# Kernel tuning notes

Hardware: AMD Instinct MI355X
Metric: run time of the kernel (lower is better)

The kernel has to match this reference:

```python
import jax, jax.numpy as jnp
import numpy as np

N_NODES = 50000
N_EDGES = 1600000
IN_DIM = 128
HID = 64
N_GRAPHS = 256


def gcn_conv(x, row, col, W, b, n_nodes):
    """PyG GCNConv: symmetric gcn_norm with self-loops, linear-then-aggregate."""
    h = x @ W  # [N, out]
    loop = jnp.arange(n_nodes, dtype=row.dtype)
    r = jnp.concatenate([row, loop])  # sources (messages from x[r])
    c = jnp.concatenate([col, loop])  # targets (aggregate at c)
    ew = jnp.ones(r.shape[0], dtype=x.dtype)
    deg = jax.ops.segment_sum(ew, c, num_segments=n_nodes)
    dinv = jnp.where(deg > 0, jax.lax.rsqrt(deg), 0.0).astype(x.dtype)
    norm = dinv[r] * dinv[c]  # [E+N]
    out = jax.ops.segment_sum(norm[:, None] * h[r], c, num_segments=n_nodes)
    return out + b


def global_mean_pool(x, batch, n_graphs):
    sums = jax.ops.segment_sum(x, batch, num_segments=n_graphs)
    cnt = jax.ops.segment_sum(jnp.ones(x.shape[0], x.dtype), batch, num_segments=n_graphs)
    return sums / jnp.clip(cnt, 1.0)[:, None]


def setup_inputs() -> dict:
    key = jax.random.key(0)
    ks = jax.random.split(key, 12)
    x = jax.random.normal(ks[0], (N_NODES, IN_DIM), dtype=jnp.float32)
    edge_index = jax.random.randint(ks[1], (2, N_EDGES), 0, N_NODES, dtype=jnp.int64)
    batch = jnp.sort(jax.random.randint(ks[2], (N_NODES,), 0, N_GRAPHS, dtype=jnp.int64))
    def glorot(k, shp):
        lim = float(np.sqrt(6.0 / (shp[0] + shp[1])))
        return jax.random.uniform(k, shp, jnp.float32, -lim, lim)
    return {
        "x": x,
        "edge_index": edge_index,
        "batch": batch,
        "W1": glorot(ks[3], (IN_DIM, HID)), "b1": jnp.zeros((HID,), jnp.float32),
        "W2": glorot(ks[4], (HID, HID)), "b2": jnp.zeros((HID,), jnp.float32),
        "W3": glorot(ks[5], (HID, HID)), "b3": jnp.zeros((HID,), jnp.float32),
        "Wl1": glorot(ks[6], (HID, 16)), "bl1": jnp.zeros((16,), jnp.float32),
        "Wl2": glorot(ks[7], (16, 1)), "bl2": jnp.zeros((1,), jnp.float32),
    }


def reference(x, edge_index, batch, W1, b1, W2, b2, W3, b3, Wl1, bl1, Wl2, bl2):
    n = x.shape[0]
    row, col = edge_index[0], edge_index[1]
    h = jax.nn.relu(gcn_conv(x, row, col, W1, b1, n))
    h = jax.nn.relu(gcn_conv(h, row, col, W2, b2, n))
    h = jax.nn.relu(gcn_conv(h, row, col, W3, b3, n))
    g = global_mean_pool(h, batch, N_GRAPHS)  # [G, 64]
    out = (g @ Wl1 + bl1) @ Wl2 + bl2  # [G, 1]
    return out
```

## Files before the change

### kernel.cpp

```cpp
#include <hip/hip_runtime.h>

#define HID 64
#define B1 256
#define NBMAX 200
#define CAP 10368

typedef __attribute__((ext_vector_type(8))) short short8;
typedef __attribute__((ext_vector_type(4))) float float4v;

__device__ __forceinline__ ushort f2bf(float f) {
  unsigned u = __float_as_uint(f);
  unsigned r = (u + 0x7fffu + ((u >> 16) & 1u)) >> 16;
  return (ushort)r;
}
__device__ __forceinline__ float bf2f(ushort v) {
  return __uint_as_float(((unsigned)v) << 16);
}
__device__ __forceinline__ float4 up4(ushort4 v) {
  float4 r;
  r.x = bf2f(v.x);
  r.y = bf2f(v.y);
  r.z = bf2f(v.z);
  r.w = bf2f(v.w);
  return r;
}


__global__ __launch_bounds__(256) void bucket_hist(const int* __restrict__ col, int E, int epb,
                                                   int* __restrict__ buckettot,
                                                   const float* __restrict__ W1,
                                                   const float* __restrict__ W2,
                                                   const float* __restrict__ W3,
                                                   ushort* __restrict__ Wt1h, ushort* __restrict__ Wt1l,
                                                   ushort* __restrict__ Wt2h, ushort* __restrict__ Wt2l,
                                                   ushort* __restrict__ Wt3h, ushort* __restrict__ Wt3l) {
  int b = blockIdx.x, t = threadIdx.x;
  int gt = b * 256 + t;
  if (gt < 128 * 64) {
    int k = gt >> 6, nn = gt & 63;
    float w = W1[gt];
    ushort h = f2bf(w);
    Wt1h[nn * 128 + k] = h;
    Wt1l[nn * 128 + k] = f2bf(w - bf2f(h));
  }
  if (gt < 64 * 64) {
    int k = gt >> 6, nn = gt & 63;
    float w2 = W2[gt], w3 = W3[gt];
    ushort h2 = f2bf(w2), h3 = f2bf(w3);
    Wt2h[nn * 64 + k] = h2;
    Wt2l[nn * 64 + k] = f2bf(w2 - bf2f(h2));
    Wt3h[nn * 64 + k] = h3;
    Wt3l[nn * 64 + k] = f2bf(w3 - bf2f(h3));
  }

  __shared__ int cnt[256];
  cnt[t] = 0;
  __syncthreads();
  int lo = b * epb, hi = min(lo + epb, E);
  for (int e = lo + t; e < hi; e += 256) atomicAdd(&cnt[col[e] >> 8], 1);
  __syncthreads();
  int v = cnt[t];
  if (v > 0) atomicAdd(&buckettot[t], v);
}

__global__ __launch_bounds__(256) void scan_buckettot(const int* __restrict__ buckettot,
                                                      int* __restrict__ bucketbase,
                                                      int* __restrict__ woffglob,
                                                      int* __restrict__ csr_off, int n, int E,
                                                      int nb) {
  __shared__ int s[256];
  int t = threadIdx.x;
  int v = (t < nb) ? buckettot[t] : 0;
  s[t] = v;
  __syncthreads();
  for (int d = 1; d < 256; d <<= 1) {
    int u = (t >= d) ? s[t - d] : 0;
    __syncthreads();
    s[t] += u;
    __syncthreads();
  }
  int base = (t == 0) ? 0 : s[t - 1];
  if (t <= nb) bucketbase[t] = base;
  woffglob[t] = base;
  if (t == 0) csr_off[n] = E;
}

__global__ __launch_bounds__(256) void bin_edges(const int* __restrict__ row,
                                                 const int* __restrict__ col, int E, int epb,
                                                 int* __restrict__ woffglob,
                                                 unsigned* __restrict__ binned) {
  __shared__ int cnt[256];
  __shared__ int ofs[256];
  __shared__ int gb[256];
  __shared__ int lcur[256];
  __shared__ unsigned stage[4096];
  int b = blockIdx.x, t = threadIdx.x;
  int lo = b * epb, hi = min(lo + epb, E);

  for (int bs = lo; bs < hi; bs += 4096) {
    int ecnt = min(4096, hi - bs);
    cnt[t] = 0;
    __syncthreads();
    for (int i = t; i < ecnt; i += 256) atomicAdd(&cnt[col[bs + i] >> 8], 1);
    __syncthreads();
    int v = cnt[t];
    ofs[t] = v;
    __syncthreads();
    for (int d = 1; d < 256; d <<= 1) {
      int u = (t >= d) ? ofs[t - d] : 0;
      __syncthreads();
      ofs[t] += u;
      __syncthreads();
    }
    int excl = ofs[t] - v;
    int g = 0;
    if (v > 0) g = atomicAdd(&woffglob[t], v);
    __syncthreads();
    ofs[t] = excl;
    gb[t] = g;
    lcur[t] = excl;
    __syncthreads();
    for (int i = t; i < ecnt; i += 256) {
      int c = col[bs + i];
      int r = row[bs + i];
      int p = atomicAdd(&lcur[c >> 8], 1);
      stage[p] = ((unsigned)r << 16) | (unsigned)c;
    }
    __syncthreads();
    for (int i = t; i < ecnt; i += 256) {
      unsigned en = stage[i];
      int bb = (en >> 8) & 255;
      binned[gb[bb] + (i - ofs[bb])] = en;
    }
    __syncthreads();
  }
}

__global__ __launch_bounds__(256) void bucket_csr(const unsigned* __restrict__ binned,
                                                  const int* __restrict__ bucketbase,
                                                  int* __restrict__ csr_off,
                                                  int* __restrict__ csr_src,
                                                  float* __restrict__ dinv, int n) {
  __shared__ int lcnt[256];
  __shared__ int lofs[256];
  __shared__ int lsrc[CAP];
  int k = blockIdx.x, t = threadIdx.x;
  int base = bucketbase[k], end = bucketbase[k + 1];
  int s = end - base;
  lcnt[t] = 0;
  __syncthreads();
  for (int i = t; i < s; i += 256) {
    unsigned p = binned[base + i];
    atomicAdd(&lcnt[p & 255u], 1);
  }
  __syncthreads();
  int v = lcnt[t];
  lofs[t] = v;
  __syncthreads();
  for (int d = 1; d < 256; d <<= 1) {
    int u = (t >= d) ? lofs[t - d] : 0;
    __syncthreads();
    lofs[t] += u;
    __syncthreads();
  }
  int excl = lofs[t] - v;
  int node = (k << 8) + t;
  if (node < n) {
    csr_off[node] = base + excl;
    dinv[node] = rsqrtf((float)(v + 1));
  }
  lcnt[t] = excl;
  __syncthreads();
  for (int i = t; i < s; i += 256) {
    unsigned p = binned[base + i];
    int pos = atomicAdd(&lcnt[p & 255u], 1);
    if (pos < CAP) lsrc[pos] = (int)(p >> 16);
  }
  __syncthreads();
  for (int i = t; i < s; i += 256) csr_src[base + i] = (i < CAP) ? lsrc[i] : 0;
}


template <int K>
__global__ __launch_bounds__(256) void gemm_mfma(const float* __restrict__ A,
                                                 const ushort* __restrict__ Wh,
                                                 const ushort* __restrict__ Wl,
                                                 const float* __restrict__ dinv,
                                                 ushort* __restrict__ out, int n) {
  int wave = (blockIdx.x * 256 + threadIdx.x) >> 6;
  int lane = threadIdx.x & 63;
  int row0 = wave * 16;
  if (row0 >= n) return;
  int m = lane & 15;
  int quad = lane >> 4;
  int r = row0 + m;
  int rc = (r < n) ? r : (n - 1);

  float4v acc[4];
#pragma unroll
  for (int t = 0; t < 4; ++t) acc[t] = (float4v){0.f, 0.f, 0.f, 0.f};

#pragma unroll
  for (int k0 = 0; k0 < K; k0 += 32) {
    const float4* xp = (const float4*)&A[(size_t)rc * K + k0 + quad * 8];
    float4 a0 = xp[0];
    float4 a1 = xp[1];
    float av[8] = {a0.x, a0.y, a0.z, a0.w, a1.x, a1.y, a1.z, a1.w};
    short8 ah, al;
#pragma unroll
    for (int i = 0; i < 8; ++i) {
      ushort h = f2bf(av[i]);
      ah[i] = (short)h;
      al[i] = (short)f2bf(av[i] - bf2f(h));
    }
#pragma unroll
    for (int t = 0; t < 4; ++t) {
      size_t wof = (size_t)(t * 16 + m) * K + k0 + quad * 8;
      short8 bh = *(const short8*)&Wh[wof];
      short8 bl = *(const short8*)&Wl[wof];
      acc[t] = __builtin_amdgcn_mfma_f32_16x16x32_bf16(ah, bh, acc[t], 0, 0, 0);
      acc[t] = __builtin_amdgcn_mfma_f32_16x16x32_bf16(al, bh, acc[t], 0, 0, 0);
      acc[t] = __builtin_amdgcn_mfma_f32_16x16x32_bf16(ah, bl, acc[t], 0, 0, 0);
    }
  }

  float4 dv = ((const float4*)dinv)[(row0 >> 2) + quad];
  float dvi[4] = {dv.x, dv.y, dv.z, dv.w};
#pragma unroll
  for (int i = 0; i < 4; ++i) {
    int orow = row0 + quad * 4 + i;
    if (orow < n) {
#pragma unroll
      for (int t = 0; t < 4; ++t) {
        out[(size_t)orow * 64 + t * 16 + m] = f2bf(dvi[i] * acc[t][i]);
      }
    }
  }
}


__global__ __launch_bounds__(256) void agg_kernel(
    const ushort* __restrict__ hs, const int* __restrict__ csr_off,
    const int* __restrict__ csr_src, const float* __restrict__ dinv,
    const float* __restrict__ bias, float* __restrict__ out, int n) {
  int wid = (blockIdx.x * 256 + threadIdx.x) >> 6;
  int lane = threadIdx.x & 63;
  if (wid >= n) return;
  int qe = lane >> 4;
  int fq = lane & 15;
  const ushort4* hs4 = (const ushort4*)hs;

  float4 acc = make_float4(0.f, 0.f, 0.f, 0.f);
  if (qe == 0) {
    float4 s = up4(hs4[(size_t)wid * 16 + fq]);
    acc.x += s.x; acc.y += s.y; acc.z += s.z; acc.w += s.w;
  }

  int j = csr_off[wid];
  int e = csr_off[wid + 1];

  int pre = min(e, (j + 3) & ~3);
  if (j + qe < pre) {
    int s0 = csr_src[j + qe];
    float4 f = up4(hs4[(size_t)s0 * 16 + fq]);
    acc.x += f.x; acc.y += f.y; acc.z += f.z; acc.w += f.w;
  }
  int base = pre;

  for (; base + 16 <= e; base += 16) {
    int4 s = *(const int4*)&csr_src[base + qe * 4];
    float4 f0 = up4(hs4[(size_t)s.x * 16 + fq]);
    float4 f1 = up4(hs4[(size_t)s.y * 16 + fq]);
    float4 f2 = up4(hs4[(size_t)s.z * 16 + fq]);
    float4 f3 = up4(hs4[(size_t)s.w * 16 + fq]);
    acc.x += f0.x + f1.x + f2.x + f3.x;
    acc.y += f0.y + f1.y + f2.y + f3.y;
    acc.z += f0.z + f1.z + f2.z + f3.z;
    acc.w += f0.w + f1.w + f2.w + f3.w;
  }

  for (; base + 4 <= e; base += 4) {
    int s0 = csr_src[base + qe];
    float4 f = up4(hs4[(size_t)s0 * 16 + fq]);
    acc.x += f.x; acc.y += f.y; acc.z += f.z; acc.w += f.w;
  }
  if (base + qe < e) {
    int s0 = csr_src[base + qe];
    float4 f = up4(hs4[(size_t)s0 * 16 + fq]);
    acc.x += f.x; acc.y += f.y; acc.z += f.z; acc.w += f.w;
  }

  acc.x += __shfl_xor(acc.x, 16, 64);
  acc.y += __shfl_xor(acc.y, 16, 64);
  acc.z += __shfl_xor(acc.z, 16, 64);
  acc.w += __shfl_xor(acc.w, 16, 64);
  acc.x += __shfl_xor(acc.x, 32, 64);
  acc.y += __shfl_xor(acc.y, 32, 64);
  acc.z += __shfl_xor(acc.z, 32, 64);
  acc.w += __shfl_xor(acc.w, 32, 64);

  if (qe == 0) {
    float d = dinv[wid];
    float4 bi = ((const float4*)bias)[fq];
    float4 r;
    r.x = fmaxf(d * acc.x + bi.x, 0.f);
    r.y = fmaxf(d * acc.y + bi.y, 0.f);
    r.z = fmaxf(d * acc.z + bi.z, 0.f);
    r.w = fmaxf(d * acc.w + bi.w, 0.f);
    ((float4*)out)[(size_t)wid * 16 + fq] = r;
  }
}


__global__ __launch_bounds__(256) void pool_mlp_kernel(
    const float* __restrict__ a, const int* __restrict__ batch, int n,
    const float* __restrict__ Wl1, const float* __restrict__ bl1,
    const float* __restrict__ Wl2, const float* __restrict__ bl2,
    float* __restrict__ out) {
  int g = blockIdx.x;
  int t = threadIdx.x;
  int lane = t & 63;
  int w = t >> 6;

  int lo = 0, hi = n;
  while (lo < hi) {
    int m = (lo + hi) >> 1;
    if (batch[m] < g) lo = m + 1; else hi = m;
  }
  int start = lo;
  lo = start; hi = n;
  while (lo < hi) {
    int m = (lo + hi) >> 1;
    if (batch[m] < g + 1) lo = m + 1; else hi = m;
  }
  int end = lo;

  float s = 0.f;
  for (int i = start + w; i < end; i += 4) s += a[i * 64 + lane];

  __shared__ float ps[4][64];
  __shared__ float gv[64];
  __shared__ float hv[16];
  ps[w][lane] = s;
  __syncthreads();
  if (w == 0) {
    float tot = ps[0][lane] + ps[1][lane] + ps[2][lane] + ps[3][lane];
    gv[lane] = tot / (float)max(end - start, 1);
  }
  __syncthreads();
  if (t < 16) {
    float h = bl1[t];
    for (int k = 0; k < 64; ++k) h += gv[k] * Wl1[k * 16 + t];
    hv[t] = h;
  }
  __syncthreads();
  if (t == 0) {
    float o = bl2[0];
    for (int j2 = 0; j2 < 16; ++j2) o += hv[j2] * Wl2[j2];
    out[g] = o;
  }
}


extern "C" void kernel_launch(void* const* d_in, const int* in_sizes, int n_in,
                              void* d_out, int out_size, void* d_ws, size_t ws_size,
                              hipStream_t stream) {
  const float* x = (const float*)d_in[0];
  const int* ei = (const int*)d_in[1];
  const int* batch = (const int*)d_in[2];
  const float* W1 = (const float*)d_in[3];
  const float* b1 = (const float*)d_in[4];
  const float* W2 = (const float*)d_in[5];
  const float* b2 = (const float*)d_in[6];
  const float* W3 = (const float*)d_in[7];
  const float* b3 = (const float*)d_in[8];
  const float* Wl1 = (const float*)d_in[9];
  const float* bl1 = (const float*)d_in[10];
  const float* Wl2 = (const float*)d_in[11];
  const float* bl2 = (const float*)d_in[12];

  int n = in_sizes[0] / 128;
  int E = in_sizes[1] / 2;
  int G = out_size;
  int nb = (n + 255) >> 8;
  int epb = (E + B1 - 1) / B1;

  const int* row = ei;
  const int* col = ei + E;

  char* p = (char*)d_ws;
  int* buckettot = (int*)p;   p += 256 * 4;
  int* bucketbase = (int*)p;  p += 272 * 4;
  int* woffglob = (int*)p;    p += 256 * 4;
  int* csr_off = (int*)p;     p += 50064 * 4;
  float* dinv = (float*)p;    p += 50016 * 4;
  ushort* Wt1h = (ushort*)p;  p += 128 * 64 * 2;
  ushort* Wt1l = (ushort*)p;  p += 128 * 64 * 2;
  ushort* Wt2h = (ushort*)p;  p += 64 * 64 * 2;
  ushort* Wt2l = (ushort*)p;  p += 64 * 64 * 2;
  ushort* Wt3h = (ushort*)p;  p += 64 * 64 * 2;
  ushort* Wt3l = (ushort*)p;  p += 64 * 64 * 2;
  int* csr_src = (int*)p;     p += (size_t)((E + 15) / 16 * 16) * 4;
  ushort* hs = (ushort*)p;    p += (size_t)n * 64 * 2;
  float* abuf = (float*)p;
  unsigned* binned = (unsigned*)hs;

  hipMemsetAsync(buckettot, 0, 256 * 4, stream);
  bucket_hist<<<B1, 256, 0, stream>>>(col, E, epb, buckettot,
                                      W1, W2, W3, Wt1h, Wt1l, Wt2h, Wt2l, Wt3h, Wt3l);
  scan_buckettot<<<1, 256, 0, stream>>>(buckettot, bucketbase, woffglob, csr_off, n, E, nb);
  bin_edges<<<B1, 256, 0, stream>>>(row, col, E, epb, woffglob, binned);
  bucket_csr<<<nb, 256, 0, stream>>>(binned, bucketbase, csr_off, csr_src, dinv, n);

  int nwaves = (n + 15) / 16;
  int gblocks = (nwaves + 3) / 4;
  int ablocks = (n * 64 + 255) / 256;

  gemm_mfma<128><<<gblocks, 256, 0, stream>>>(x, Wt1h, Wt1l, dinv, hs, n);
  agg_kernel<<<ablocks, 256, 0, stream>>>(hs, csr_off, csr_src, dinv, b1, abuf, n);
  gemm_mfma<64><<<gblocks, 256, 0, stream>>>(abuf, Wt2h, Wt2l, dinv, hs, n);
  agg_kernel<<<ablocks, 256, 0, stream>>>(hs, csr_off, csr_src, dinv, b2, abuf, n);
  gemm_mfma<64><<<gblocks, 256, 0, stream>>>(abuf, Wt3h, Wt3l, dinv, hs, n);
  agg_kernel<<<ablocks, 256, 0, stream>>>(hs, csr_off, csr_src, dinv, b3, abuf, n);
  pool_mlp_kernel<<<G, 256, 0, stream>>>(abuf, batch, n, Wl1, bl1, Wl2, bl2, (float*)d_out);
}
```

Measured before the change: 332.1 us.

## Split feature table into column halves for cache-resident gathers; fuse pooling into aggregation

The GEMM now writes the bf16 hidden features as two 32-column half tables, and each aggregation layer runs as two passes, one per half. Each half table (about 3.2 MB) is more likely to stay in L2/LLC during the random neighbor gather. The last layer's aggregation also atomically adds into per-graph sums, so the separate pooling pass over the full activation buffer goes away. The cost is reading the CSR structure twice per layer, extra launches, and float atomic contention on only 256 graph rows.

```diff
diff --git a/kernel.cpp b/kernel.cpp
--- a/kernel.cpp
+++ b/kernel.cpp
@@ -186,7 +186,8 @@
                                                  const ushort* __restrict__ Wh,
                                                  const ushort* __restrict__ Wl,
                                                  const float* __restrict__ dinv,
-                                                 ushort* __restrict__ out, int n) {
+                                                 ushort* __restrict__ hsA,
+                                                 ushort* __restrict__ hsB, int n) {
   int wave = (blockIdx.x * 256 + threadIdx.x) >> 6;
   int lane = threadIdx.x & 63;
   int row0 = wave * 16;
@@ -230,66 +231,67 @@
   for (int i = 0; i < 4; ++i) {
     int orow = row0 + quad * 4 + i;
     if (orow < n) {
-#pragma unroll
-      for (int t = 0; t < 4; ++t) {
-        out[(size_t)orow * 64 + t * 16 + m] = f2bf(dvi[i] * acc[t][i]);
-      }
-    }
-  }
-}
-
-
-__global__ __launch_bounds__(256) void agg_kernel(
-    const ushort* __restrict__ hs, const int* __restrict__ csr_off,
+      hsA[(size_t)orow * 32 + 0 * 16 + m] = f2bf(dvi[i] * acc[0][i]);
+      hsA[(size_t)orow * 32 + 1 * 16 + m] = f2bf(dvi[i] * acc[1][i]);
+      hsB[(size_t)orow * 32 + 0 * 16 + m] = f2bf(dvi[i] * acc[2][i]);
+      hsB[(size_t)orow * 32 + 1 * 16 + m] = f2bf(dvi[i] * acc[3][i]);
+    }
+  }
+}
+
+
+template <int MODE>
+__global__ __launch_bounds__(256) void agg_half(
+    const ushort* __restrict__ hsH, const int* __restrict__ csr_off,
     const int* __restrict__ csr_src, const float* __restrict__ dinv,
-    const float* __restrict__ bias, float* __restrict__ out, int n) {
+    const float* __restrict__ bias,
+    float* __restrict__ out,
+    int colOff,
+    const int* __restrict__ batch, float* __restrict__ gsum, int n) {
   int wid = (blockIdx.x * 256 + threadIdx.x) >> 6;
   int lane = threadIdx.x & 63;
   if (wid >= n) return;
-  int qe = lane >> 4;
-  int fq = lane & 15;
-  const ushort4* hs4 = (const ushort4*)hs;
+  int grp = lane >> 3;
+  int fq = lane & 7;
+  const ushort4* h4 = (const ushort4*)hsH;
 
   float4 acc = make_float4(0.f, 0.f, 0.f, 0.f);
-  if (qe == 0) {
-    float4 s = up4(hs4[(size_t)wid * 16 + fq]);
-    acc.x += s.x; acc.y += s.y; acc.z += s.z; acc.w += s.w;
+  if (grp == 0) {
+    acc = up4(h4[(size_t)wid * 8 + fq]);
   }
 
   int j = csr_off[wid];
   int e = csr_off[wid + 1];
-
-  int pre = min(e, (j + 3) & ~3);
-  if (j + qe < pre) {
-    int s0 = csr_src[j + qe];
-    float4 f = up4(hs4[(size_t)s0 * 16 + fq]);
-    acc.x += f.x; acc.y += f.y; acc.z += f.z; acc.w += f.w;
-  }
-  int base = pre;
-
-  for (; base + 16 <= e; base += 16) {
-    int4 s = *(const int4*)&csr_src[base + qe * 4];
-    float4 f0 = up4(hs4[(size_t)s.x * 16 + fq]);
-    float4 f1 = up4(hs4[(size_t)s.y * 16 + fq]);
-    float4 f2 = up4(hs4[(size_t)s.z * 16 + fq]);
-    float4 f3 = up4(hs4[(size_t)s.w * 16 + fq]);
+  int base = j;
+  for (; base + 32 <= e; base += 32) {
+    int s0 = csr_src[base + grp];
+    int s1 = csr_src[base + 8 + grp];
+    int s2 = csr_src[base + 16 + grp];
+    int s3 = csr_src[base + 24 + grp];
+    float4 f0 = up4(h4[(size_t)s0 * 8 + fq]);
+    float4 f1 = up4(h4[(size_t)s1 * 8 + fq]);
+    float4 f2 = up4(h4[(size_t)s2 * 8 + fq]);
+    float4 f3 = up4(h4[(size_t)s3 * 8 + fq]);
     acc.x += f0.x + f1.x + f2.x + f3.x;
     acc.y += f0.y + f1.y + f2.y + f3.y;
     acc.z += f0.z + f1.z + f2.z + f3.z;
     acc.w += f0.w + f1.w + f2.w + f3.w;
   }
-
-  for (; base + 4 <= e; base += 4) {
-    int s0 = csr_src[base + qe];
-    float4 f = up4(hs4[(size_t)s0 * 16 + fq]);
+  for (; base + 8 <= e; base += 8) {
+    int s0 = csr_src[base + grp];
+    float4 f = up4(h4[(size_t)s0 * 8 + fq]);
     acc.x += f.x; acc.y += f.y; acc.z += f.z; acc.w += f.w;
   }
-  if (base + qe < e) {
-    int s0 = csr_src[base + qe];
-    float4 f = up4(hs4[(size_t)s0 * 16 + fq]);
+  if (base + grp < e) {
+    int s0 = csr_src[base + grp];
+    float4 f = up4(h4[(size_t)s0 * 8 + fq]);
     acc.x += f.x; acc.y += f.y; acc.z += f.z; acc.w += f.w;
   }
 
+  acc.x += __shfl_xor(acc.x, 8, 64);
+  acc.y += __shfl_xor(acc.y, 8, 64);
+  acc.z += __shfl_xor(acc.z, 8, 64);
+  acc.w += __shfl_xor(acc.w, 8, 64);
   acc.x += __shfl_xor(acc.x, 16, 64);
   acc.y += __shfl_xor(acc.y, 16, 64);
   acc.z += __shfl_xor(acc.z, 16, 64);
@@ -299,7 +301,7 @@
   acc.z += __shfl_xor(acc.z, 32, 64);
   acc.w += __shfl_xor(acc.w, 32, 64);
 
-  if (qe == 0) {
+  if (grp == 0) {
     float d = dinv[wid];
     float4 bi = ((const float4*)bias)[fq];
     float4 r;
@@ -307,20 +309,27 @@
     r.y = fmaxf(d * acc.y + bi.y, 0.f);
     r.z = fmaxf(d * acc.z + bi.z, 0.f);
     r.w = fmaxf(d * acc.w + bi.w, 0.f);
-    ((float4*)out)[(size_t)wid * 16 + fq] = r;
-  }
-}
-
-
-__global__ __launch_bounds__(256) void pool_mlp_kernel(
-    const float* __restrict__ a, const int* __restrict__ batch, int n,
+    if (MODE == 0) {
+      ((float4*)out)[(size_t)wid * 16 + colOff + fq] = r;
+    } else {
+      int g = batch[wid];
+      float* gp = &gsum[(size_t)g * 64 + (colOff + fq) * 4];
+      atomicAdd(gp + 0, r.x);
+      atomicAdd(gp + 1, r.y);
+      atomicAdd(gp + 2, r.z);
+      atomicAdd(gp + 3, r.w);
+    }
+  }
+}
+
+
+__global__ __launch_bounds__(64) void mlp_kernel(
+    const float* __restrict__ gsum, const int* __restrict__ batch, int n,
     const float* __restrict__ Wl1, const float* __restrict__ bl1,
     const float* __restrict__ Wl2, const float* __restrict__ bl2,
     float* __restrict__ out) {
   int g = blockIdx.x;
-  int t = threadIdx.x;
-  int lane = t & 63;
-  int w = t >> 6;
+  int lane = threadIdx.x;
 
   int lo = 0, hi = n;
   while (lo < hi) {
@@ -335,26 +344,19 @@
   }
   int end = lo;
 
-  float s = 0.f;
-  for (int i = start + w; i < end; i += 4) s += a[i * 64 + lane];
-
-  __shared__ float ps[4][64];
+  float mean = gsum[(size_t)g * 64 + lane] / (float)max(end - start, 1);
+
   __shared__ float gv[64];
   __shared__ float hv[16];
-  ps[w][lane] = s;
-  __syncthreads();
-  if (w == 0) {
-    float tot = ps[0][lane] + ps[1][lane] + ps[2][lane] + ps[3][lane];
-    gv[lane] = tot / (float)max(end - start, 1);
-  }
-  __syncthreads();
-  if (t < 16) {
-    float h = bl1[t];
-    for (int k = 0; k < 64; ++k) h += gv[k] * Wl1[k * 16 + t];
-    hv[t] = h;
-  }
-  __syncthreads();
-  if (t == 0) {
+  gv[lane] = mean;
+  __syncthreads();
+  if (lane < 16) {
+    float h = bl1[lane];
+    for (int k = 0; k < 64; ++k) h += gv[k] * Wl1[k * 16 + lane];
+    hv[lane] = h;
+  }
+  __syncthreads();
+  if (lane == 0) {
     float o = bl2[0];
     for (int j2 = 0; j2 < 16; ++j2) o += hv[j2] * Wl2[j2];
     out[g] = o;
@@ -390,6 +392,7 @@
 
   char* p = (char*)d_ws;
   int* buckettot = (int*)p;   p += 256 * 4;
+  float* gsum = (float*)p;    p += 256 * 64 * 4;
   int* bucketbase = (int*)p;  p += 272 * 4;
   int* woffglob = (int*)p;    p += 256 * 4;
   int* csr_off = (int*)p;     p += 50064 * 4;
@@ -401,11 +404,12 @@
   ushort* Wt3h = (ushort*)p;  p += 64 * 64 * 2;
   ushort* Wt3l = (ushort*)p;  p += 64 * 64 * 2;
   int* csr_src = (int*)p;     p += (size_t)((E + 15) / 16 * 16) * 4;
-  ushort* hs = (ushort*)p;    p += (size_t)n * 64 * 2;
+  ushort* hsA = (ushort*)p;   p += (size_t)n * 32 * 2;
+  ushort* hsB = (ushort*)p;   p += (size_t)n * 32 * 2;
   float* abuf = (float*)p;
-  unsigned* binned = (unsigned*)hs;
-
-  hipMemsetAsync(buckettot, 0, 256 * 4, stream);
+  unsigned* binned = (unsigned*)hsA;
+
+  hipMemsetAsync(buckettot, 0, (256 + 256 * 64) * 4, stream);
   bucket_hist<<<B1, 256, 0, stream>>>(col, E, epb, buckettot,
                                       W1, W2, W3, Wt1h, Wt1l, Wt2h, Wt2l, Wt3h, Wt3l);
   scan_buckettot<<<1, 256, 0, stream>>>(buckettot, bucketbase, woffglob, csr_off, n, E, nb);
@@ -416,11 +420,14 @@
   int gblocks = (nwaves + 3) / 4;
   int ablocks = (n * 64 + 255) / 256;
 
-  gemm_mfma<128><<<gblocks, 256, 0, stream>>>(x, Wt1h, Wt1l, dinv, hs, n);
-  agg_kernel<<<ablocks, 256, 0, stream>>>(hs, csr_off, csr_src, dinv, b1, abuf, n);
-  gemm_mfma<64><<<gblocks, 256, 0, stream>>>(abuf, Wt2h, Wt2l, dinv, hs, n);
-  agg_kernel<<<ablocks, 256, 0, stream>>>(hs, csr_off, csr_src, dinv, b2, abuf, n);
-  gemm_mfma<64><<<gblocks, 256, 0, stream>>>(abuf, Wt3h, Wt3l, dinv, hs, n);
-  agg_kernel<<<ablocks, 256, 0, stream>>>(hs, csr_off, csr_src, dinv, b3, abuf, n);
-  pool_mlp_kernel<<<G, 256, 0, stream>>>(abuf, batch, n, Wl1, bl1, Wl2, bl2, (float*)d_out);
-}
+  gemm_mfma<128><<<gblocks, 256, 0, stream>>>(x, Wt1h, Wt1l, dinv, hsA, hsB, n);
+  agg_half<0><<<ablocks, 256, 0, stream>>>(hsA, csr_off, csr_src, dinv, b1, abuf, 0, batch, gsum, n);
+  agg_half<0><<<ablocks, 256, 0, stream>>>(hsB, csr_off, csr_src, dinv, b1 + 32, abuf, 8, batch, gsum, n);
+  gemm_mfma<64><<<gblocks, 256, 0, stream>>>(abuf, Wt2h, Wt2l, dinv, hsA, hsB, n);
+  agg_half<0><<<ablocks, 256, 0, stream>>>(hsA, csr_off, csr_src, dinv, b2, abuf, 0, batch, gsum, n);
+  agg_half<0><<<ablocks, 256, 0, stream>>>(hsB, csr_off, csr_src, dinv, b2 + 32, abuf, 8, batch, gsum, n);
+  gemm_mfma<64><<<gblocks, 256, 0, stream>>>(abuf, Wt3h, Wt3l, dinv, hsA, hsB, n);
+  agg_half<1><<<ablocks, 256, 0, stream>>>(hsA, csr_off, csr_src, dinv, b3, abuf, 0, batch, gsum, n);
+  agg_half<1><<<ablocks, 256, 0, stream>>>(hsB, csr_off, csr_src, dinv, b3 + 32, abuf, 8, batch, gsum, n);
+  mlp_kernel<<<G, 64, 0, stream>>>(gsum, batch, n, Wl1, bl1, Wl2, bl2, (float*)d_out);
+}
```

Result: slower. 442.9 us (+33.4%).

## Fuse whole GCN pipeline into one persistent cooperative kernel with grid syncs

Applied to the files above, without the earlier changes.

Replaces the chain of separate launches (histogram, scan, binning, CSR build, three GEMM/aggregate pairs, pooling) with a single cooperative persistent kernel. Phases are separated by grid.sync and loops are grid-strided over a grid sized from occupancy. The last aggregation phase appears to accumulate per-graph sums into gsum so pooling skips a separate pass over the activations, and the aggregate loop is unrolled to gather 32 edges at a time. This removes launch gaps and intermediate kernel boundaries, at the cost of grid-wide barriers, a shared-memory union that may limit occupancy, and a smaller CAP for the CSR staging buffer.

```diff
diff --git a/kernel.cpp b/kernel.cpp
--- a/kernel.cpp
+++ b/kernel.cpp
@@ -1,9 +1,10 @@
 #include <hip/hip_runtime.h>
-
-#define HID 64
-#define B1 256
-#define NBMAX 200
-#define CAP 10368
+#include <hip/hip_cooperative_groups.h>
+
+namespace cg = cooperative_groups;
+
+#define TPB 256
+#define CAP 8960
 
 typedef __attribute__((ext_vector_type(8))) short short8;
 typedef __attribute__((ext_vector_type(4))) float float4v;
@@ -25,339 +26,374 @@
   return r;
 }
 
-
-__global__ __launch_bounds__(256) void bucket_hist(const int* __restrict__ col, int E, int epb,
-                                                   int* __restrict__ buckettot,
-                                                   const float* __restrict__ W1,
-                                                   const float* __restrict__ W2,
-                                                   const float* __restrict__ W3,
-                                                   ushort* __restrict__ Wt1h, ushort* __restrict__ Wt1l,
-                                                   ushort* __restrict__ Wt2h, ushort* __restrict__ Wt2l,
-                                                   ushort* __restrict__ Wt3h, ushort* __restrict__ Wt3l) {
-  int b = blockIdx.x, t = threadIdx.x;
-  int gt = b * 256 + t;
-  if (gt < 128 * 64) {
-    int k = gt >> 6, nn = gt & 63;
-    float w = W1[gt];
-    ushort h = f2bf(w);
-    Wt1h[nn * 128 + k] = h;
-    Wt1l[nn * 128 + k] = f2bf(w - bf2f(h));
-  }
-  if (gt < 64 * 64) {
-    int k = gt >> 6, nn = gt & 63;
-    float w2 = W2[gt], w3 = W3[gt];
-    ushort h2 = f2bf(w2), h3 = f2bf(w3);
-    Wt2h[nn * 64 + k] = h2;
-    Wt2l[nn * 64 + k] = f2bf(w2 - bf2f(h2));
-    Wt3h[nn * 64 + k] = h3;
-    Wt3l[nn * 64 + k] = f2bf(w3 - bf2f(h3));
-  }
-
-  __shared__ int cnt[256];
-  cnt[t] = 0;
-  __syncthreads();
-  int lo = b * epb, hi = min(lo + epb, E);
-  for (int e = lo + t; e < hi; e += 256) atomicAdd(&cnt[col[e] >> 8], 1);
-  __syncthreads();
-  int v = cnt[t];
-  if (v > 0) atomicAdd(&buckettot[t], v);
-}
-
-__global__ __launch_bounds__(256) void scan_buckettot(const int* __restrict__ buckettot,
-                                                      int* __restrict__ bucketbase,
-                                                      int* __restrict__ woffglob,
-                                                      int* __restrict__ csr_off, int n, int E,
-                                                      int nb) {
-  __shared__ int s[256];
-  int t = threadIdx.x;
-  int v = (t < nb) ? buckettot[t] : 0;
-  s[t] = v;
-  __syncthreads();
-  for (int d = 1; d < 256; d <<= 1) {
-    int u = (t >= d) ? s[t - d] : 0;
-    __syncthreads();
-    s[t] += u;
-    __syncthreads();
-  }
-  int base = (t == 0) ? 0 : s[t - 1];
-  if (t <= nb) bucketbase[t] = base;
-  woffglob[t] = base;
-  if (t == 0) csr_off[n] = E;
-}
-
-__global__ __launch_bounds__(256) void bin_edges(const int* __restrict__ row,
-                                                 const int* __restrict__ col, int E, int epb,
-                                                 int* __restrict__ woffglob,
-                                                 unsigned* __restrict__ binned) {
-  __shared__ int cnt[256];
-  __shared__ int ofs[256];
-  __shared__ int gb[256];
-  __shared__ int lcur[256];
-  __shared__ unsigned stage[4096];
-  int b = blockIdx.x, t = threadIdx.x;
-  int lo = b * epb, hi = min(lo + epb, E);
-
-  for (int bs = lo; bs < hi; bs += 4096) {
-    int ecnt = min(4096, hi - bs);
-    cnt[t] = 0;
-    __syncthreads();
-    for (int i = t; i < ecnt; i += 256) atomicAdd(&cnt[col[bs + i] >> 8], 1);
-    __syncthreads();
-    int v = cnt[t];
-    ofs[t] = v;
-    __syncthreads();
-    for (int d = 1; d < 256; d <<= 1) {
-      int u = (t >= d) ? ofs[t - d] : 0;
-      __syncthreads();
-      ofs[t] += u;
-      __syncthreads();
-    }
-    int excl = ofs[t] - v;
-    int g = 0;
-    if (v > 0) g = atomicAdd(&woffglob[t], v);
-    __syncthreads();
-    ofs[t] = excl;
-    gb[t] = g;
-    lcur[t] = excl;
-    __syncthreads();
-    for (int i = t; i < ecnt; i += 256) {
-      int c = col[bs + i];
-      int r = row[bs + i];
-      int p = atomicAdd(&lcur[c >> 8], 1);
-      stage[p] = ((unsigned)r << 16) | (unsigned)c;
-    }
-    __syncthreads();
-    for (int i = t; i < ecnt; i += 256) {
-      unsigned en = stage[i];
-      int bb = (en >> 8) & 255;
-      binned[gb[bb] + (i - ofs[bb])] = en;
-    }
-    __syncthreads();
-  }
-}
-
-__global__ __launch_bounds__(256) void bucket_csr(const unsigned* __restrict__ binned,
-                                                  const int* __restrict__ bucketbase,
-                                                  int* __restrict__ csr_off,
-                                                  int* __restrict__ csr_src,
-                                                  float* __restrict__ dinv, int n) {
-  __shared__ int lcnt[256];
-  __shared__ int lofs[256];
-  __shared__ int lsrc[CAP];
-  int k = blockIdx.x, t = threadIdx.x;
-  int base = bucketbase[k], end = bucketbase[k + 1];
-  int s = end - base;
-  lcnt[t] = 0;
-  __syncthreads();
-  for (int i = t; i < s; i += 256) {
-    unsigned p = binned[base + i];
-    atomicAdd(&lcnt[p & 255u], 1);
-  }
-  __syncthreads();
-  int v = lcnt[t];
-  lofs[t] = v;
-  __syncthreads();
-  for (int d = 1; d < 256; d <<= 1) {
-    int u = (t >= d) ? lofs[t - d] : 0;
-    __syncthreads();
-    lofs[t] += u;
-    __syncthreads();
-  }
-  int excl = lofs[t] - v;
-  int node = (k << 8) + t;
-  if (node < n) {
-    csr_off[node] = base + excl;
-    dinv[node] = rsqrtf((float)(v + 1));
-  }
-  lcnt[t] = excl;
-  __syncthreads();
-  for (int i = t; i < s; i += 256) {
-    unsigned p = binned[base + i];
-    int pos = atomicAdd(&lcnt[p & 255u], 1);
-    if (pos < CAP) lsrc[pos] = (int)(p >> 16);
-  }
-  __syncthreads();
-  for (int i = t; i < s; i += 256) csr_src[base + i] = (i < CAP) ? lsrc[i] : 0;
-}
-
+struct GcnP {
+  const float* x;
+  const int* row;
+  const int* col;
+  const int* batch;
+  const float* W1; const float* b1;
+  const float* W2; const float* b2;
+  const float* W3; const float* b3;
+  const float* Wl1; const float* bl1;
+  const float* Wl2; const float* bl2;
+  float* out;
+  int n, E, G, nb, epb;
+  int* buckettot; int* bucketbase; int* woffglob; int* csr_off;
+  float* dinv;
+  ushort *Wt1h, *Wt1l, *Wt2h, *Wt2l, *Wt3h, *Wt3l;
+  int* csr_src;
+  unsigned* binned;
+  ushort* hs;
+  float* abuf;
+  float* gsum;
+};
+
+union Sh {
+  struct { int cnt[256]; int ofs[256]; int gb[256]; int lcur[256]; unsigned stage[4096]; } bin;
+  struct { int lcnt[256]; int lofs[256]; int lsrc[CAP]; } csr;
+  struct { float gv[64]; float hv[16]; } pool;
+  int hist[256];
+  int scan[256];
+};
 
 template <int K>
-__global__ __launch_bounds__(256) void gemm_mfma(const float* __restrict__ A,
-                                                 const ushort* __restrict__ Wh,
-                                                 const ushort* __restrict__ Wl,
-                                                 const float* __restrict__ dinv,
-                                                 ushort* __restrict__ out, int n) {
-  int wave = (blockIdx.x * 256 + threadIdx.x) >> 6;
+__device__ __forceinline__ void gemm_phase(const float* __restrict__ A,
+                                           const ushort* __restrict__ Wh,
+                                           const ushort* __restrict__ Wl,
+                                           const float* __restrict__ dinv,
+                                           ushort* __restrict__ out, int n) {
+  int nw = gridDim.x * (TPB / 64);
+  int gw = (blockIdx.x * TPB + threadIdx.x) >> 6;
   int lane = threadIdx.x & 63;
-  int row0 = wave * 16;
-  if (row0 >= n) return;
   int m = lane & 15;
   int quad = lane >> 4;
-  int r = row0 + m;
-  int rc = (r < n) ? r : (n - 1);
-
-  float4v acc[4];
-#pragma unroll
-  for (int t = 0; t < 4; ++t) acc[t] = (float4v){0.f, 0.f, 0.f, 0.f};
-
-#pragma unroll
-  for (int k0 = 0; k0 < K; k0 += 32) {
-    const float4* xp = (const float4*)&A[(size_t)rc * K + k0 + quad * 8];
-    float4 a0 = xp[0];
-    float4 a1 = xp[1];
-    float av[8] = {a0.x, a0.y, a0.z, a0.w, a1.x, a1.y, a1.z, a1.w};
-    short8 ah, al;
-#pragma unroll
-    for (int i = 0; i < 8; ++i) {
-      ushort h = f2bf(av[i]);
-      ah[i] = (short)h;
-      al[i] = (short)f2bf(av[i] - bf2f(h));
-    }
-#pragma unroll
-    for (int t = 0; t < 4; ++t) {
-      size_t wof = (size_t)(t * 16 + m) * K + k0 + quad * 8;
-      short8 bh = *(const short8*)&Wh[wof];
-      short8 bl = *(const short8*)&Wl[wof];
-      acc[t] = __builtin_amdgcn_mfma_f32_16x16x32_bf16(ah, bh, acc[t], 0, 0, 0);
-      acc[t] = __builtin_amdgcn_mfma_f32_16x16x32_bf16(al, bh, acc[t], 0, 0, 0);
-      acc[t] = __builtin_amdgcn_mfma_f32_16x16x32_bf16(ah, bl, acc[t], 0, 0, 0);
-    }
-  }
-
-  float4 dv = ((const float4*)dinv)[(row0 >> 2) + quad];
-  float dvi[4] = {dv.x, dv.y, dv.z, dv.w};
-#pragma unroll
-  for (int i = 0; i < 4; ++i) {
-    int orow = row0 + quad * 4 + i;
-    if (orow < n) {
+  int ntiles = (n + 15) >> 4;
+  for (int tile = gw; tile < ntiles; tile += nw) {
+    int row0 = tile << 4;
+    int r = row0 + m;
+    int rc = (r < n) ? r : (n - 1);
+
+    float4v acc[4];
+#pragma unroll
+    for (int t = 0; t < 4; ++t) acc[t] = (float4v){0.f, 0.f, 0.f, 0.f};
+
+#pragma unroll
+    for (int k0 = 0; k0 < K; k0 += 32) {
+      const float4* xp = (const float4*)&A[(size_t)rc * K + k0 + quad * 8];
+      float4 a0 = xp[0];
+      float4 a1 = xp[1];
+      float av[8] = {a0.x, a0.y, a0.z, a0.w, a1.x, a1.y, a1.z, a1.w};
+      short8 ah, al;
+#pragma unroll
+      for (int i = 0; i < 8; ++i) {
+        ushort h = f2bf(av[i]);
+        ah[i] = (short)h;
+        al[i] = (short)f2bf(av[i] - bf2f(h));
+      }
 #pragma unroll
       for (int t = 0; t < 4; ++t) {
-        out[(size_t)orow * 64 + t * 16 + m] = f2bf(dvi[i] * acc[t][i]);
-      }
-    }
-  }
-}
-
-
-__global__ __launch_bounds__(256) void agg_kernel(
-    const ushort* __restrict__ hs, const int* __restrict__ csr_off,
-    const int* __restrict__ csr_src, const float* __restrict__ dinv,
-    const float* __restrict__ bias, float* __restrict__ out, int n) {
-  int wid = (blockIdx.x * 256 + threadIdx.x) >> 6;
+        size_t wof = (size_t)(t * 16 + m) * K + k0 + quad * 8;
+        short8 bh = *(const short8*)&Wh[wof];
+        short8 bl = *(const short8*)&Wl[wof];
+        acc[t] = __builtin_amdgcn_mfma_f32_16x16x32_bf16(ah, bh, acc[t], 0, 0, 0);
+        acc[t] = __builtin_amdgcn_mfma_f32_16x16x32_bf16(al, bh, acc[t], 0, 0, 0);
+        acc[t] = __builtin_amdgcn_mfma_f32_16x16x32_bf16(ah, bl, acc[t], 0, 0, 0);
+      }
+    }
+
+    float4 dv = ((const float4*)dinv)[(row0 >> 2) + quad];
+    float dvi[4] = {dv.x, dv.y, dv.z, dv.w};
+#pragma unroll
+    for (int i = 0; i < 4; ++i) {
+      int orow = row0 + quad * 4 + i;
+      if (orow < n) {
+#pragma unroll
+        for (int t = 0; t < 4; ++t) {
+          out[(size_t)orow * 64 + t * 16 + m] = f2bf(dvi[i] * acc[t][i]);
+        }
+      }
+    }
+  }
+}
+
+template <int MODE>
+__device__ __forceinline__ void agg_phase(const ushort* __restrict__ hs,
+                                          const int* __restrict__ csr_off,
+                                          const int* __restrict__ csr_src,
+                                          const float* __restrict__ dinv,
+                                          const float* __restrict__ bias,
+                                          float* __restrict__ out,
+                                          const int* __restrict__ batch,
+                                          float* __restrict__ gsum, int n) {
+  int nw = gridDim.x * (TPB / 64);
+  int gw = (blockIdx.x * TPB + threadIdx.x) >> 6;
   int lane = threadIdx.x & 63;
-  if (wid >= n) return;
   int qe = lane >> 4;
   int fq = lane & 15;
   const ushort4* hs4 = (const ushort4*)hs;
 
-  float4 acc = make_float4(0.f, 0.f, 0.f, 0.f);
-  if (qe == 0) {
-    float4 s = up4(hs4[(size_t)wid * 16 + fq]);
-    acc.x += s.x; acc.y += s.y; acc.z += s.z; acc.w += s.w;
-  }
-
-  int j = csr_off[wid];
-  int e = csr_off[wid + 1];
-
-  int pre = min(e, (j + 3) & ~3);
-  if (j + qe < pre) {
-    int s0 = csr_src[j + qe];
-    float4 f = up4(hs4[(size_t)s0 * 16 + fq]);
-    acc.x += f.x; acc.y += f.y; acc.z += f.z; acc.w += f.w;
-  }
-  int base = pre;
-
-  for (; base + 16 <= e; base += 16) {
-    int4 s = *(const int4*)&csr_src[base + qe * 4];
-    float4 f0 = up4(hs4[(size_t)s.x * 16 + fq]);
-    float4 f1 = up4(hs4[(size_t)s.y * 16 + fq]);
-    float4 f2 = up4(hs4[(size_t)s.z * 16 + fq]);
-    float4 f3 = up4(hs4[(size_t)s.w * 16 + fq]);
-    acc.x += f0.x + f1.x + f2.x + f3.x;
-    acc.y += f0.y + f1.y + f2.y + f3.y;
-    acc.z += f0.z + f1.z + f2.z + f3.z;
-    acc.w += f0.w + f1.w + f2.w + f3.w;
-  }
-
-  for (; base + 4 <= e; base += 4) {
-    int s0 = csr_src[base + qe];
-    float4 f = up4(hs4[(size_t)s0 * 16 + fq]);
-    acc.x += f.x; acc.y += f.y; acc.z += f.z; acc.w += f.w;
-  }
-  if (base + qe < e) {
-    int s0 = csr_src[base + qe];
-    float4 f = up4(hs4[(size_t)s0 * 16 + fq]);
-    acc.x += f.x; acc.y += f.y; acc.z += f.z; acc.w += f.w;
-  }
-
-  acc.x += __shfl_xor(acc.x, 16, 64);
-  acc.y += __shfl_xor(acc.y, 16, 64);
-  acc.z += __shfl_xor(acc.z, 16, 64);
-  acc.w += __shfl_xor(acc.w, 16, 64);
-  acc.x += __shfl_xor(acc.x, 32, 64);
-  acc.y += __shfl_xor(acc.y, 32, 64);
-  acc.z += __shfl_xor(acc.z, 32, 64);
-  acc.w += __shfl_xor(acc.w, 32, 64);
-
-  if (qe == 0) {
-    float d = dinv[wid];
-    float4 bi = ((const float4*)bias)[fq];
-    float4 r;
-    r.x = fmaxf(d * acc.x + bi.x, 0.f);
-    r.y = fmaxf(d * acc.y + bi.y, 0.f);
-    r.z = fmaxf(d * acc.z + bi.z, 0.f);
-    r.w = fmaxf(d * acc.w + bi.w, 0.f);
-    ((float4*)out)[(size_t)wid * 16 + fq] = r;
-  }
-}
-
-
-__global__ __launch_bounds__(256) void pool_mlp_kernel(
-    const float* __restrict__ a, const int* __restrict__ batch, int n,
-    const float* __restrict__ Wl1, const float* __restrict__ bl1,
-    const float* __restrict__ Wl2, const float* __restrict__ bl2,
-    float* __restrict__ out) {
-  int g = blockIdx.x;
-  int t = threadIdx.x;
-  int lane = t & 63;
-  int w = t >> 6;
-
-  int lo = 0, hi = n;
-  while (lo < hi) {
-    int m = (lo + hi) >> 1;
-    if (batch[m] < g) lo = m + 1; else hi = m;
-  }
-  int start = lo;
-  lo = start; hi = n;
-  while (lo < hi) {
-    int m = (lo + hi) >> 1;
-    if (batch[m] < g + 1) lo = m + 1; else hi = m;
-  }
-  int end = lo;
-
-  float s = 0.f;
-  for (int i = start + w; i < end; i += 4) s += a[i * 64 + lane];
-
-  __shared__ float ps[4][64];
-  __shared__ float gv[64];
-  __shared__ float hv[16];
-  ps[w][lane] = s;
-  __syncthreads();
-  if (w == 0) {
-    float tot = ps[0][lane] + ps[1][lane] + ps[2][lane] + ps[3][lane];
-    gv[lane] = tot / (float)max(end - start, 1);
-  }
-  __syncthreads();
-  if (t < 16) {
-    float h = bl1[t];
-    for (int k = 0; k < 64; ++k) h += gv[k] * Wl1[k * 16 + t];
-    hv[t] = h;
-  }
-  __syncthreads();
-  if (t == 0) {
-    float o = bl2[0];
-    for (int j2 = 0; j2 < 16; ++j2) o += hv[j2] * Wl2[j2];
-    out[g] = o;
+  for (int wid = gw; wid < n; wid += nw) {
+    float4 acc = make_float4(0.f, 0.f, 0.f, 0.f);
+    if (qe == 0) {
+      acc = up4(hs4[(size_t)wid * 16 + fq]);
+    }
+    int j = csr_off[wid];
+    int e = csr_off[wid + 1];
+
+    int pre = min(e, (j + 3) & ~3);
+    if (j + qe < pre) {
+      int s0 = csr_src[j + qe];
+      float4 f = up4(hs4[(size_t)s0 * 16 + fq]);
+      acc.x += f.x; acc.y += f.y; acc.z += f.z; acc.w += f.w;
+    }
+    int base = pre;
+
+    for (; base + 32 <= e; base += 32) {
+      int4 sa = *(const int4*)&csr_src[base + qe * 4];
+      int4 sb = *(const int4*)&csr_src[base + 16 + qe * 4];
+      float4 f0 = up4(hs4[(size_t)sa.x * 16 + fq]);
+      float4 f1 = up4(hs4[(size_t)sa.y * 16 + fq]);
+      float4 f2 = up4(hs4[(size_t)sa.z * 16 + fq]);
+      float4 f3 = up4(hs4[(size_t)sa.w * 16 + fq]);
+      float4 f4 = up4(hs4[(size_t)sb.x * 16 + fq]);
+      float4 f5 = up4(hs4[(size_t)sb.y * 16 + fq]);
+      float4 f6 = up4(hs4[(size_t)sb.z * 16 + fq]);
+      float4 f7 = up4(hs4[(size_t)sb.w * 16 + fq]);
+      acc.x += (f0.x + f1.x) + (f2.x + f3.x) + ((f4.x + f5.x) + (f6.x + f7.x));
+      acc.y += (f0.y + f1.y) + (f2.y + f3.y) + ((f4.y + f5.y) + (f6.y + f7.y));
+      acc.z += (f0.z + f1.z) + (f2.z + f3.z) + ((f4.z + f5.z) + (f6.z + f7.z));
+      acc.w += (f0.w + f1.w) + (f2.w + f3.w) + ((f4.w + f5.w) + (f6.w + f7.w));
+    }
+    for (; base + 16 <= e; base += 16) {
+      int4 s = *(const int4*)&csr_src[base + qe * 4];
+      float4 f0 = up4(hs4[(size_t)s.x * 16 + fq]);
+      float4 f1 = up4(hs4[(size_t)s.y * 16 + fq]);
+      float4 f2 = up4(hs4[(size_t)s.z * 16 + fq]);
+      float4 f3 = up4(hs4[(size_t)s.w * 16 + fq]);
+      acc.x += f0.x + f1.x + f2.x + f3.x;
+      acc.y += f0.y + f1.y + f2.y + f3.y;
+      acc.z += f0.z + f1.z + f2.z + f3.z;
+      acc.w += f0.w + f1.w + f2.w + f3.w;
+    }
+    for (; base + 4 <= e; base += 4) {
+      int s0 = csr_src[base + qe];
+      float4 f = up4(hs4[(size_t)s0 * 16 + fq]);
+      acc.x += f.x; acc.y += f.y; acc.z += f.z; acc.w += f.w;
+    }
+    if (base + qe < e) {
+      int s0 = csr_src[base + qe];
+      float4 f = up4(hs4[(size_t)s0 * 16 + fq]);
+      acc.x += f.x; acc.y += f.y; acc.z += f.z; acc.w += f.w;
+    }
+
+    acc.x += __shfl_xor(acc.x, 16, 64);
+    acc.y += __shfl_xor(acc.y, 16, 64);
+    acc.z += __shfl_xor(acc.z, 16, 64);
+    acc.w += __shfl_xor(acc.w, 16, 64);
+    acc.x += __shfl_xor(acc.x, 32, 64);
+    acc.y += __shfl_xor(acc.y, 32, 64);
+    acc.z += __shfl_xor(acc.z, 32, 64);
+    acc.w += __shfl_xor(acc.w, 32, 64);
+
+    if (qe == 0) {
+      float d = dinv[wid];
+      float4 bi = ((const float4*)bias)[fq];
+      float4 r;
+      r.x = fmaxf(d * acc.x + bi.x, 0.f);
+      r.y = fmaxf(d * acc.y + bi.y, 0.f);
+      r.z = fmaxf(d * acc.z + bi.z, 0.f);
+      r.w = fmaxf(d * acc.w + bi.w, 0.f);
+      if (MODE == 0) {
+        ((float4*)out)[(size_t)wid * 16 + fq] = r;
+      } else {
+        int g = batch[wid];
+        float* gp = &gsum[(size_t)g * 64 + fq * 4];
+        atomicAdd(gp + 0, r.x);
+        atomicAdd(gp + 1, r.y);
+        atomicAdd(gp + 2, r.z);
+        atomicAdd(gp + 3, r.w);
+      }
+    }
+  }
+}
+
+__global__ __launch_bounds__(TPB, 3) void fused_gcn(GcnP p) {
+  cg::grid_group grid = cg::this_grid();
+  __shared__ Sh sh;
+  int b = blockIdx.x, t = threadIdx.x;
+  int gt = b * TPB + t;
+  int gsz = gridDim.x * TPB;
+
+  if (gt < 256) p.buckettot[gt] = 0;
+  for (int i = gt; i < 256 * 64; i += gsz) p.gsum[i] = 0.f;
+  if (gt < 128 * 64) {
+    int k = gt >> 6, nn = gt & 63;
+    float w = p.W1[gt];
+    ushort h = f2bf(w);
+    p.Wt1h[nn * 128 + k] = h;
+    p.Wt1l[nn * 128 + k] = f2bf(w - bf2f(h));
+  }
+  if (gt < 64 * 64) {
+    int k = gt >> 6, nn = gt & 63;
+    float w2 = p.W2[gt], w3 = p.W3[gt];
+    ushort h2 = f2bf(w2), h3 = f2bf(w3);
+    p.Wt2h[nn * 64 + k] = h2;
+    p.Wt2l[nn * 64 + k] = f2bf(w2 - bf2f(h2));
+    p.Wt3h[nn * 64 + k] = h3;
+    p.Wt3l[nn * 64 + k] = f2bf(w3 - bf2f(h3));
+  }
+  grid.sync();
+
+  {
+    sh.hist[t] = 0;
+    __syncthreads();
+    int lo = b * p.epb, hi = min(lo + p.epb, p.E);
+    for (int e = lo + t; e < hi; e += TPB) atomicAdd(&sh.hist[p.col[e] >> 8], 1);
+    __syncthreads();
+    int v = sh.hist[t];
+    if (v > 0) atomicAdd(&p.buckettot[t], v);
+  }
+  grid.sync();
+
+  if (b == 0) {
+    int v = (t < p.nb) ? p.buckettot[t] : 0;
+    sh.scan[t] = v;
+    __syncthreads();
+    for (int d = 1; d < 256; d <<= 1) {
+      int u = (t >= d) ? sh.scan[t - d] : 0;
+      __syncthreads();
+      sh.scan[t] += u;
+      __syncthreads();
+    }
+    int base = (t == 0) ? 0 : sh.scan[t - 1];
+    if (t <= p.nb) p.bucketbase[t] = base;
+    p.woffglob[t] = base;
+    if (t == 0) p.csr_off[p.n] = p.E;
+  }
+  grid.sync();
+
+  {
+    int lo = b * p.epb, hi = min(lo + p.epb, p.E);
+    for (int bs = lo; bs < hi; bs += 4096) {
+      int ecnt = min(4096, hi - bs);
+      sh.bin.cnt[t] = 0;
+      __syncthreads();
+      for (int i = t; i < ecnt; i += TPB) atomicAdd(&sh.bin.cnt[p.col[bs + i] >> 8], 1);
+      __syncthreads();
+      int v = sh.bin.cnt[t];
+      sh.bin.ofs[t] = v;
+      __syncthreads();
+      for (int d = 1; d < 256; d <<= 1) {
+        int u = (t >= d) ? sh.bin.ofs[t - d] : 0;
+        __syncthreads();
+        sh.bin.ofs[t] += u;
+        __syncthreads();
+      }
+      int excl = sh.bin.ofs[t] - v;
+      int g = 0;
+      if (v > 0) g = atomicAdd(&p.woffglob[t], v);
+      __syncthreads();
+      sh.bin.ofs[t] = excl;
+      sh.bin.gb[t] = g;
+      sh.bin.lcur[t] = excl;
+      __syncthreads();
+      for (int i = t; i < ecnt; i += TPB) {
+        int c = p.col[bs + i];
+        int r = p.row[bs + i];
+        int pos = atomicAdd(&sh.bin.lcur[c >> 8], 1);
+        sh.bin.stage[pos] = ((unsigned)r << 16) | (unsigned)c;
+      }
+      __syncthreads();
+      for (int i = t; i < ecnt; i += TPB) {
+        unsigned en = sh.bin.stage[i];
+        int bb = (en >> 8) & 255;
+        p.binned[sh.bin.gb[bb] + (i - sh.bin.ofs[bb])] = en;
+      }
+      __syncthreads();
+    }
+  }
+  grid.sync();
+
+  for (int k = b; k < p.nb; k += gridDim.x) {
+    int base = p.bucketbase[k], end = p.bucketbase[k + 1];
+    int s = end - base;
+    sh.csr.lcnt[t] = 0;
+    __syncthreads();
+    for (int i = t; i < s; i += TPB) {
+      unsigned e2 = p.binned[base + i];
+      atomicAdd(&sh.csr.lcnt[e2 & 255u], 1);
+    }
+    __syncthreads();
+    int v = sh.csr.lcnt[t];
+    sh.csr.lofs[t] = v;
+    __syncthreads();
+    for (int d = 1; d < 256; d <<= 1) {
+      int u = (t >= d) ? sh.csr.lofs[t - d] : 0;
+      __syncthreads();
+      sh.csr.lofs[t] += u;
+      __syncthreads();
+    }
+    int excl = sh.csr.lofs[t] - v;
+    int node = (k << 8) + t;
+    if (node < p.n) {
+      p.csr_off[node] = base + excl;
+      p.dinv[node] = rsqrtf((float)(v + 1));
+    }
+    sh.csr.lcnt[t] = excl;
+    __syncthreads();
+    for (int i = t; i < s; i += TPB) {
+      unsigned e2 = p.binned[base + i];
+      int pos = atomicAdd(&sh.csr.lcnt[e2 & 255u], 1);
+      if (pos < CAP) sh.csr.lsrc[pos] = (int)(e2 >> 16);
+    }
+    __syncthreads();
+    for (int i = t; i < s; i += TPB) p.csr_src[base + i] = (i < CAP) ? sh.csr.lsrc[i] : 0;
+    __syncthreads();
+  }
+  grid.sync();
+
+  gemm_phase<128>(p.x, p.Wt1h, p.Wt1l, p.dinv, p.hs, p.n);
+  grid.sync();
+  agg_phase<0>(p.hs, p.csr_off, p.csr_src, p.dinv, p.b1, p.abuf, p.batch, p.gsum, p.n);
+  grid.sync();
+  gemm_phase<64>(p.abuf, p.Wt2h, p.Wt2l, p.dinv, p.hs, p.n);
+  grid.sync();
+  agg_phase<0>(p.hs, p.csr_off, p.csr_src, p.dinv, p.b2, p.abuf, p.batch, p.gsum, p.n);
+  grid.sync();
+  gemm_phase<64>(p.abuf, p.Wt3h, p.Wt3l, p.dinv, p.hs, p.n);
+  grid.sync();
+  agg_phase<1>(p.hs, p.csr_off, p.csr_src, p.dinv, p.b3, p.abuf, p.batch, p.gsum, p.n);
+  grid.sync();
+
+  if (b < p.G) {
+    int g = b;
+    if (t < 64) {
+      int lo = 0, hi = p.n;
+      while (lo < hi) {
+        int m = (lo + hi) >> 1;
+        if (p.batch[m] < g) lo = m + 1; else hi = m;
+      }
+      int start = lo;
+      lo = start; hi = p.n;
+      while (lo < hi) {
+        int m = (lo + hi) >> 1;
+        if (p.batch[m] < g + 1) lo = m + 1; else hi = m;
+      }
+      int end = lo;
+      sh.pool.gv[t] = p.gsum[(size_t)g * 64 + t] / (float)max(end - start, 1);
+    }
+    __syncthreads();
+    if (t < 16) {
+      float h = p.bl1[t];
+      for (int k = 0; k < 64; ++k) h += sh.pool.gv[k] * p.Wl1[k * 16 + t];
+      sh.pool.hv[t] = h;
+    }
+    __syncthreads();
+    if (t == 0) {
+      float o = p.bl2[0];
+      for (int j2 = 0; j2 < 16; ++j2) o += sh.pool.hv[j2] * p.Wl2[j2];
+      p.out[g] = o;
+    }
   }
 }
 
@@ -365,62 +401,51 @@
 extern "C" void kernel_launch(void* const* d_in, const int* in_sizes, int n_in,
                               void* d_out, int out_size, void* d_ws, size_t ws_size,
                               hipStream_t stream) {
-  const float* x = (const float*)d_in[0];
+  GcnP p;
+  p.x = (const float*)d_in[0];
   const int* ei = (const int*)d_in[1];
-  const int* batch = (const int*)d_in[2];
-  const float* W1 = (const float*)d_in[3];
-  const float* b1 = (const float*)d_in[4];
-  const float* W2 = (const float*)d_in[5];
-  const float* b2 = (const float*)d_in[6];
-  const float* W3 = (const float*)d_in[7];
-  const float* b3 = (const float*)d_in[8];
-  const float* Wl1 = (const float*)d_in[9];
-  const float* bl1 = (const float*)d_in[10];
-  const float* Wl2 = (const float*)d_in[11];
-  const float* bl2 = (const float*)d_in[12];
-
-  int n = in_sizes[0] / 128;
-  int E = in_sizes[1] / 2;
-  int G = out_size;
-  int nb = (n + 255) >> 8;
-  int epb = (E + B1 - 1) / B1;
-
-  const int* row = ei;
-  const int* col = ei + E;
-
-  char* p = (char*)d_ws;
-  int* buckettot = (int*)p;   p += 256 * 4;
-  int* bucketbase = (int*)p;  p += 272 * 4;
-  int* woffglob = (int*)p;    p += 256 * 4;
-  int* csr_off = (int*)p;     p += 50064 * 4;
-  float* dinv = (float*)p;    p += 50016 * 4;
-  ushort* Wt1h = (ushort*)p;  p += 128 * 64 * 2;
-  ushort* Wt1l = (ushort*)p;  p += 128 * 64 * 2;
-  ushort* Wt2h = (ushort*)p;  p += 64 * 64 * 2;
-  ushort* Wt2l = (ushort*)p;  p += 64 * 64 * 2;
-  ushort* Wt3h = (ushort*)p;  p += 64 * 64 * 2;
-  ushort* Wt3l = (ushort*)p;  p += 64 * 64 * 2;
-  int* csr_src = (int*)p;     p += (size_t)((E + 15) / 16 * 16) * 4;
-  ushort* hs = (ushort*)p;    p += (size_t)n * 64 * 2;
-  float* abuf = (float*)p;
-  unsigned* binned = (unsigned*)hs;
-
-  hipMemsetAsync(buckettot, 0, 256 * 4, stream);
-  bucket_hist<<<B1, 256, 0, stream>>>(col, E, epb, buckettot,
-                                      W1, W2, W3, Wt1h, Wt1l, Wt2h, Wt2l, Wt3h, Wt3l);
-  scan_buckettot<<<1, 256, 0, stream>>>(buckettot, bucketbase, woffglob, csr_off, n, E, nb);
-  bin_edges<<<B1, 256, 0, stream>>>(row, col, E, epb, woffglob, binned);
-  bucket_csr<<<nb, 256, 0, stream>>>(binned, bucketbase, csr_off, csr_src, dinv, n);
-
-  int nwaves = (n + 15) / 16;
-  int gblocks = (nwaves + 3) / 4;
-  int ablocks = (n * 64 + 255) / 256;
-
-  gemm_mfma<128><<<gblocks, 256, 0, stream>>>(x, Wt1h, Wt1l, dinv, hs, n);
-  agg_kernel<<<ablocks, 256, 0, stream>>>(hs, csr_off, csr_src, dinv, b1, abuf, n);
-  gemm_mfma<64><<<gblocks, 256, 0, stream>>>(abuf, Wt2h, Wt2l, dinv, hs, n);
-  agg_kernel<<<ablocks, 256, 0, stream>>>(hs, csr_off, csr_src, dinv, b2, abuf, n);
-  gemm_mfma<64><<<gblocks, 256, 0, stream>>>(abuf, Wt3h, Wt3l, dinv, hs, n);
-  agg_kernel<<<ablocks, 256, 0, stream>>>(hs, csr_off, csr_src, dinv, b3, abuf, n);
-  pool_mlp_kernel<<<G, 256, 0, stream>>>(abuf, batch, n, Wl1, bl1, Wl2, bl2, (float*)d_out);
-}
+  p.batch = (const int*)d_in[2];
+  p.W1 = (const float*)d_in[3];  p.b1 = (const float*)d_in[4];
+  p.W2 = (const float*)d_in[5];  p.b2 = (const float*)d_in[6];
+  p.W3 = (const float*)d_in[7];  p.b3 = (const float*)d_in[8];
+  p.Wl1 = (const float*)d_in[9]; p.bl1 = (const float*)d_in[10];
+  p.Wl2 = (const float*)d_in[11]; p.bl2 = (const float*)d_in[12];
+  p.out = (float*)d_out;
+
+  p.n = in_sizes[0] / 128;
+  p.E = in_sizes[1] / 2;
+  p.G = out_size;
+  p.nb = (p.n + 255) >> 8;
+
+  int maxB = 0;
+  if (hipOccupancyMaxActiveBlocksPerMultiprocessor(&maxB, fused_gcn, TPB, 0) != hipSuccess ||
+      maxB < 1)
+    maxB = 1;
+  if (maxB > 4) maxB = 4;
+  int grid = maxB * 256;
+  p.epb = (p.E + grid - 1) / grid;
+
+  p.row = ei;
+  p.col = ei + p.E;
+
+  char* q = (char*)d_ws;
+  p.buckettot = (int*)q;   q += 256 * 4;
+  p.gsum = (float*)q;      q += 256 * 64 * 4;
+  p.bucketbase = (int*)q;  q += 272 * 4;
+  p.woffglob = (int*)q;    q += 256 * 4;
+  p.csr_off = (int*)q;     q += 50064 * 4;
+  p.dinv = (float*)q;      q += 50016 * 4;
+  p.Wt1h = (ushort*)q;     q += 128 * 64 * 2;
+  p.Wt1l = (ushort*)q;     q += 128 * 64 * 2;
+  p.Wt2h = (ushort*)q;     q += 64 * 64 * 2;
+  p.Wt2l = (ushort*)q;     q += 64 * 64 * 2;
+  p.Wt3h = (ushort*)q;     q += 64 * 64 * 2;
+  p.Wt3l = (ushort*)q;     q += 64 * 64 * 2;
+  p.csr_src = (int*)q;     q += (size_t)((p.E + 15) / 16 * 16) * 4;
+  p.hs = (ushort*)q;       q += (size_t)p.n * 64 * 2;
+  p.abuf = (float*)q;
+  p.binned = (unsigned*)p.hs;
+
+  void* args[] = {(void*)&p};
+  hipLaunchCooperativeKernel(fused_gcn, dim3(grid), dim3(TPB), args, 0, stream);
+}
```

New measurement: 1.028 ms. 210% more time.
